# Performance work log

Measured on AMD Instinct MI355X. Metric: run time of the kernel, lower is better.

The kernel has to match this reference:

```python
import jax, jax.numpy as jnp
import numpy as np

N_NODES = 100000
N_EDGES = 3200000  # avg degree 32
D_IN = 128
D_OUT = 64
BN_EPS = 0.001


def setup_inputs() -> dict:
    key = jax.random.key(0)
    k1, k2, k3, k4, k5 = jax.random.split(key, 5)
    x = jax.random.normal(k1, (N_NODES, D_IN), dtype=jnp.float32)
    W = jax.random.normal(k2, (D_IN, D_OUT), dtype=jnp.float32) * 0.05
    edge_val = jax.random.uniform(k3, (N_EDGES,), dtype=jnp.float32)
    edge_src = jax.random.randint(k4, (N_EDGES,), 0, N_NODES, dtype=jnp.int32)
    edge_dst = jax.random.randint(k5, (N_EDGES,), 0, N_NODES, dtype=jnp.int32)
    return {"x": x, "W": W, "edge_val": edge_val,
            "edge_src": edge_src, "edge_dst": edge_dst}


def reference(x, W, edge_val, edge_src, edge_dst):
    # pre_sup = X @ W  (dense feature transform; dropout rate is 0 -> identity)
    pre_sup = x @ W  # [N, D_OUT]
    # support = A @ pre_sup, A given in COO form: A[dst, src] = edge_val
    msgs = edge_val[:, None] * pre_sup[edge_src]          # [E, D_OUT]
    out = jax.ops.segment_sum(msgs, edge_dst, num_segments=N_NODES)  # [N, D_OUT]
    # tf.nn.moments over all-but-last axis + batch_norm (no scale/offset, eps=1e-3)
    mean = jnp.mean(out, axis=0)
    var = jnp.var(out, axis=0)
    out = (out - mean) * jax.lax.rsqrt(var + BN_EPS)
    return jax.nn.relu(out)
```

## Files before the change

kernel.cpp:

```cpp
#include <hip/hip_runtime.h>
#include <stdint.h>

#define D_IN  128
#define D_OUT 64
#define BN_EPS 1e-3f

#define BIN_SHIFT 6
#define BIN_NODES 64
#define BIN_CAP   2560
#define CHUNK     8192
#define MAX_BINS  1600
#define STAT_SLICES 64

typedef __attribute__((ext_vector_type(8))) short bf16x8;
typedef __attribute__((ext_vector_type(4))) float f32x4;

__device__ __forceinline__ ushort f32_to_bf16_rne(float f) {
  uint u = __float_as_uint(f);
  u += 0x7FFFu + ((u >> 16) & 1u);
  return (ushort)(u >> 16);
}
__device__ __forceinline__ float bf16_to_f32(ushort h) {
  return __uint_as_float((uint)h << 16);
}

__global__ __launch_bounds__(256) void gemm_mfma_kernel(
    const float* __restrict__ x, const float* __restrict__ W,
    ushort* __restrict__ pre16, int n_nodes, int n_tiles) {
  __shared__ ushort Wb[D_IN * D_OUT];
  const int t = threadIdx.x;
  for (int i = t; i < D_IN * D_OUT; i += 256) Wb[i] = f32_to_bf16_rne(W[i]);
  __syncthreads();

  const int lane = t & 63;
  const int wave = t >> 6;
  const int m = lane & 15;
  const int quad = lane >> 4;

  bf16x8 bfrag[4][4];
#pragma unroll
  for (int nt = 0; nt < 4; ++nt)
#pragma unroll
    for (int s = 0; s < 4; ++s)
#pragma unroll
      for (int j = 0; j < 8; ++j)
        bfrag[nt][s][j] =
            (short)Wb[(32 * s + quad * 8 + j) * D_OUT + nt * 16 + m];

  for (int tile = blockIdx.x; tile < n_tiles; tile += gridDim.x) {
    const int rbase = tile * 64 + wave * 16;
    const int row = rbase + m;
    const size_t rl = (size_t)min(row, n_nodes - 1);
    f32x4 acc0 = {0.f, 0.f, 0.f, 0.f}, acc1 = {0.f, 0.f, 0.f, 0.f};
    f32x4 acc2 = {0.f, 0.f, 0.f, 0.f}, acc3 = {0.f, 0.f, 0.f, 0.f};
#pragma unroll
    for (int s = 0; s < 4; ++s) {
      const float4 xa = *(const float4*)&x[rl * D_IN + s * 32 + quad * 8];
      const float4 xb = *(const float4*)&x[rl * D_IN + s * 32 + quad * 8 + 4];
      bf16x8 af;
      af[0] = (short)f32_to_bf16_rne(xa.x);
      af[1] = (short)f32_to_bf16_rne(xa.y);
      af[2] = (short)f32_to_bf16_rne(xa.z);
      af[3] = (short)f32_to_bf16_rne(xa.w);
      af[4] = (short)f32_to_bf16_rne(xb.x);
      af[5] = (short)f32_to_bf16_rne(xb.y);
      af[6] = (short)f32_to_bf16_rne(xb.z);
      af[7] = (short)f32_to_bf16_rne(xb.w);
      acc0 = __builtin_amdgcn_mfma_f32_16x16x32_bf16(af, bfrag[0][s], acc0, 0, 0, 0);
      acc1 = __builtin_amdgcn_mfma_f32_16x16x32_bf16(af, bfrag[1][s], acc1, 0, 0, 0);
      acc2 = __builtin_amdgcn_mfma_f32_16x16x32_bf16(af, bfrag[2][s], acc2, 0, 0, 0);
      acc3 = __builtin_amdgcn_mfma_f32_16x16x32_bf16(af, bfrag[3][s], acc3, 0, 0, 0);
    }
#pragma unroll
    for (int reg = 0; reg < 4; ++reg) {
      const int r = rbase + quad * 4 + reg;
      if (r < n_nodes) {
        ushort* po = &pre16[(size_t)r * D_OUT + m];
        po[0]  = f32_to_bf16_rne(acc0[reg]);
        po[16] = f32_to_bf16_rne(acc1[reg]);
        po[32] = f32_to_bf16_rne(acc2[reg]);
        po[48] = f32_to_bf16_rne(acc3[reg]);
      }
    }
  }
}

__global__ __launch_bounds__(256) void partition_kernel(
    const float* __restrict__ ev, const int* __restrict__ esrc,
    const int* __restrict__ edst, int* __restrict__ bin_cursor,
    uint2* __restrict__ bucket, int n_edges, int n_bins) {
  __shared__ int cnt[MAX_BINS];
  __shared__ int base[MAX_BINS];
  const int t = threadIdx.x;
  const int beg = blockIdx.x * CHUNK;
  const int end = min(beg + CHUNK, n_edges);

  for (int i = t; i < n_bins; i += 256) cnt[i] = 0;
  __syncthreads();

  for (int i = beg + t * 4; i < end; i += 1024) {
    if (i + 3 < end) {
      const int4 d4 = *(const int4*)&edst[i];
      atomicAdd(&cnt[d4.x >> BIN_SHIFT], 1);
      atomicAdd(&cnt[d4.y >> BIN_SHIFT], 1);
      atomicAdd(&cnt[d4.z >> BIN_SHIFT], 1);
      atomicAdd(&cnt[d4.w >> BIN_SHIFT], 1);
    } else {
      for (int k = i; k < end; ++k) atomicAdd(&cnt[edst[k] >> BIN_SHIFT], 1);
    }
  }
  __syncthreads();

  for (int i = t; i < n_bins; i += 256) {
    const int c = cnt[i];
    int b = 0;
    if (c > 0) b = atomicAdd(&bin_cursor[i], c);
    if (b > BIN_CAP) b = BIN_CAP;
    base[i] = i * BIN_CAP + b;
    cnt[i] = 0;
  }
  __syncthreads();

  for (int i = beg + t * 4; i < end; i += 1024) {
    if (i + 3 < end) {
      const int4 d4 = *(const int4*)&edst[i];
      const int4 s4 = *(const int4*)&esrc[i];
      const float4 v4 = *(const float4*)&ev[i];
#pragma unroll
      for (int k = 0; k < 4; ++k) {
        const int dst = (&d4.x)[k];
        const int src = (&s4.x)[k];
        const float v = (&v4.x)[k];
        const int bin = dst >> BIN_SHIFT;
        const int r = atomicAdd(&cnt[bin], 1);
        const int pos = base[bin] + r;
        if (pos < (bin + 1) * BIN_CAP) {
          const uint w0 = ((uint)(dst & (BIN_NODES - 1)) << 17) | (uint)src;
          bucket[pos] = make_uint2(w0, __float_as_uint(v));
        }
      }
    } else {
      for (int k = i; k < end; ++k) {
        const int dst = edst[k];
        const int bin = dst >> BIN_SHIFT;
        const int r = atomicAdd(&cnt[bin], 1);
        const int pos = base[bin] + r;
        if (pos < (bin + 1) * BIN_CAP) {
          const uint w0 = ((uint)(dst & (BIN_NODES - 1)) << 17) | (uint)esrc[k];
          bucket[pos] = make_uint2(w0, __float_as_uint(ev[k]));
        }
      }
    }
  }
}

__global__ __launch_bounds__(256) void bin_sort_kernel(
    uint2* __restrict__ bucket, const int* __restrict__ bin_cursor,
    int2* __restrict__ seg, int n_nodes) {
  __shared__ uint s_src[BIN_CAP];
  __shared__ uint s_val[BIN_CAP];
  __shared__ int s_hist[BIN_NODES];
  __shared__ int s_off[BIN_NODES + 1];
  __shared__ int s_cur[BIN_NODES];

  const int t = threadIdx.x;
  const int bin = blockIdx.x;
  const int cnt = min(bin_cursor[bin], BIN_CAP);
  const int64_t rbase = (int64_t)bin * BIN_CAP;

  if (t < BIN_NODES) s_hist[t] = 0;
  __syncthreads();

  for (int i = t; i < cnt; i += 256)
    atomicAdd(&s_hist[bucket[rbase + i].x >> 17], 1);
  __syncthreads();

  int own = (t < BIN_NODES) ? s_hist[t] : 0;
  for (int off = 1; off < BIN_NODES; off <<= 1) {
    int u = 0;
    if (t < BIN_NODES && t >= off) u = s_hist[t - off];
    __syncthreads();
    if (t < BIN_NODES) s_hist[t] += u;
    __syncthreads();
  }
  if (t < BIN_NODES) {
    const int e = s_hist[t] - own;
    s_off[t] = e;
    s_cur[t] = e;
  }
  if (t == 0) s_off[BIN_NODES] = cnt;
  __syncthreads();

  for (int i = t; i < cnt; i += 256) {
    const uint2 r = bucket[rbase + i];
    const int d = r.x >> 17;
    const int p = atomicAdd(&s_cur[d], 1);
    s_src[p] = r.x & 0x1FFFFu;
    s_val[p] = r.y;
  }
  __syncthreads();

  for (int i = t; i < cnt; i += 256)
    bucket[rbase + i] = make_uint2(s_src[i], s_val[i]);

  if (t < BIN_NODES) {
    const int node = bin * BIN_NODES + t;
    if (node < n_nodes)
      seg[node] = make_int2((int)rbase + s_off[t], (int)rbase + s_off[t + 1]);
  }
}

__global__ __launch_bounds__(256) void gather_kernel(
    const ushort* __restrict__ pre16, const uint2* __restrict__ srec,
    const int2* __restrict__ seg, float* __restrict__ out,
    float* __restrict__ stats, int n_nodes) {
  __shared__ float red[4 * 64];
  __shared__ float red2[4 * 64];

  const int t = threadIdx.x;
  const int lane = t & 63;
  const int wave = t >> 6;
  const int half = lane >> 5;
  const int hl = lane & 31;
  const int node = blockIdx.x * 4 + wave;
  float csx = 0.f, csy = 0.f, cs2x = 0.f, cs2y = 0.f;

  if (node < n_nodes) {
    const int2 se = seg[node];
    const int je = se.y;
    float a0x = 0.f, a0y = 0.f, a1x = 0.f, a1y = 0.f;
    float a2x = 0.f, a2y = 0.f, a3x = 0.f, a3y = 0.f;
    float a4x = 0.f, a4y = 0.f, a5x = 0.f, a5y = 0.f;
    float a6x = 0.f, a6y = 0.f, a7x = 0.f, a7y = 0.f;
    int j = se.x + half;
    for (; j + 14 < je; j += 16) {
      const uint2 r0 = srec[j],      r1 = srec[j + 2];
      const uint2 r2 = srec[j + 4],  r3 = srec[j + 6];
      const uint2 r4 = srec[j + 8],  r5 = srec[j + 10];
      const uint2 r6 = srec[j + 12], r7 = srec[j + 14];
      const uint p0 = *(const uint*)&pre16[(size_t)r0.x * D_OUT + 2 * hl];
      const uint p1 = *(const uint*)&pre16[(size_t)r1.x * D_OUT + 2 * hl];
      const uint p2 = *(const uint*)&pre16[(size_t)r2.x * D_OUT + 2 * hl];
      const uint p3 = *(const uint*)&pre16[(size_t)r3.x * D_OUT + 2 * hl];
      const uint p4 = *(const uint*)&pre16[(size_t)r4.x * D_OUT + 2 * hl];
      const uint p5 = *(const uint*)&pre16[(size_t)r5.x * D_OUT + 2 * hl];
      const uint p6 = *(const uint*)&pre16[(size_t)r6.x * D_OUT + 2 * hl];
      const uint p7 = *(const uint*)&pre16[(size_t)r7.x * D_OUT + 2 * hl];
      const float v0 = __uint_as_float(r0.y), v1 = __uint_as_float(r1.y);
      const float v2 = __uint_as_float(r2.y), v3 = __uint_as_float(r3.y);
      const float v4 = __uint_as_float(r4.y), v5 = __uint_as_float(r5.y);
      const float v6 = __uint_as_float(r6.y), v7 = __uint_as_float(r7.y);
      a0x += v0 * bf16_to_f32((ushort)(p0 & 0xFFFFu));
      a0y += v0 * bf16_to_f32((ushort)(p0 >> 16));
      a1x += v1 * bf16_to_f32((ushort)(p1 & 0xFFFFu));
      a1y += v1 * bf16_to_f32((ushort)(p1 >> 16));
      a2x += v2 * bf16_to_f32((ushort)(p2 & 0xFFFFu));
      a2y += v2 * bf16_to_f32((ushort)(p2 >> 16));
      a3x += v3 * bf16_to_f32((ushort)(p3 & 0xFFFFu));
      a3y += v3 * bf16_to_f32((ushort)(p3 >> 16));
      a4x += v4 * bf16_to_f32((ushort)(p4 & 0xFFFFu));
      a4y += v4 * bf16_to_f32((ushort)(p4 >> 16));
      a5x += v5 * bf16_to_f32((ushort)(p5 & 0xFFFFu));
      a5y += v5 * bf16_to_f32((ushort)(p5 >> 16));
      a6x += v6 * bf16_to_f32((ushort)(p6 & 0xFFFFu));
      a6y += v6 * bf16_to_f32((ushort)(p6 >> 16));
      a7x += v7 * bf16_to_f32((ushort)(p7 & 0xFFFFu));
      a7y += v7 * bf16_to_f32((ushort)(p7 >> 16));
    }
    for (; j + 6 < je; j += 8) {
      const uint2 r0 = srec[j],     r1 = srec[j + 2];
      const uint2 r2 = srec[j + 4], r3 = srec[j + 6];
      const uint p0 = *(const uint*)&pre16[(size_t)r0.x * D_OUT + 2 * hl];
      const uint p1 = *(const uint*)&pre16[(size_t)r1.x * D_OUT + 2 * hl];
      const uint p2 = *(const uint*)&pre16[(size_t)r2.x * D_OUT + 2 * hl];
      const uint p3 = *(const uint*)&pre16[(size_t)r3.x * D_OUT + 2 * hl];
      const float v0 = __uint_as_float(r0.y), v1 = __uint_as_float(r1.y);
      const float v2 = __uint_as_float(r2.y), v3 = __uint_as_float(r3.y);
      a0x += v0 * bf16_to_f32((ushort)(p0 & 0xFFFFu));
      a0y += v0 * bf16_to_f32((ushort)(p0 >> 16));
      a1x += v1 * bf16_to_f32((ushort)(p1 & 0xFFFFu));
      a1y += v1 * bf16_to_f32((ushort)(p1 >> 16));
      a2x += v2 * bf16_to_f32((ushort)(p2 & 0xFFFFu));
      a2y += v2 * bf16_to_f32((ushort)(p2 >> 16));
      a3x += v3 * bf16_to_f32((ushort)(p3 & 0xFFFFu));
      a3y += v3 * bf16_to_f32((ushort)(p3 >> 16));
    }
    for (; j < je; j += 2) {
      const uint2 r = srec[j];
      const float v = __uint_as_float(r.y);
      const uint p = *(const uint*)&pre16[(size_t)r.x * D_OUT + 2 * hl];
      a0x += v * bf16_to_f32((ushort)(p & 0xFFFFu));
      a0y += v * bf16_to_f32((ushort)(p >> 16));
    }
    float ax = ((a0x + a1x) + (a2x + a3x)) + ((a4x + a5x) + (a6x + a7x));
    float ay = ((a0y + a1y) + (a2y + a3y)) + ((a4y + a5y) + (a6y + a7y));
    ax += __shfl_xor(ax, 32);
    ay += __shfl_xor(ay, 32);
    if (half == 0) {
      *(float2*)&out[(size_t)node * D_OUT + 2 * hl] = make_float2(ax, ay);
      csx = ax;
      cs2x = ax * ax;
      csy = ay;
      cs2y = ay * ay;
    }
  }

  if (half == 0) {
    red[wave * 64 + 2 * hl] = csx;
    red[wave * 64 + 2 * hl + 1] = csy;
    red2[wave * 64 + 2 * hl] = cs2x;
    red2[wave * 64 + 2 * hl + 1] = cs2y;
  }
  __syncthreads();
  if (t < 64) {
    const float s = red[t] + red[64 + t] + red[128 + t] + red[192 + t];
    const float s2 = red2[t] + red2[64 + t] + red2[128 + t] + red2[192 + t];
    const int sl = (blockIdx.x & (STAT_SLICES - 1)) * 128;
    atomicAdd(&stats[sl + t], s);
    atomicAdd(&stats[sl + 64 + t], s2);
  }
}

__global__ __launch_bounds__(128) void stats_reduce_kernel(
    const float* __restrict__ stats, float* __restrict__ sfinal) {
  const int c = threadIdx.x;
  float s = 0.f;
#pragma unroll 8
  for (int sl = 0; sl < STAT_SLICES; ++sl) s += stats[sl * 128 + c];
  sfinal[c] = s;
}

__global__ __launch_bounds__(256) void norm_kernel(
    float* __restrict__ out, const float* __restrict__ stats, int64_t n_vec4,
    float inv_n) {
  const int c = (threadIdx.x * 4) & 63;
  float mean[4], scale[4];
#pragma unroll
  for (int k = 0; k < 4; ++k) {
    mean[k] = stats[c + k] * inv_n;
    const float var = stats[64 + c + k] * inv_n - mean[k] * mean[k];
    scale[k] = rsqrtf(var + BN_EPS);
  }
  const int64_t stride = (int64_t)gridDim.x * 256;
  for (int64_t i = (int64_t)blockIdx.x * 256 + threadIdx.x; i < n_vec4;
       i += stride) {
    float4 v = ((float4*)out)[i];
    v.x = (v.x - mean[0]) * scale[0];
    v.y = (v.y - mean[1]) * scale[1];
    v.z = (v.z - mean[2]) * scale[2];
    v.w = (v.w - mean[3]) * scale[3];
    v.x = v.x > 0.f ? v.x : 0.f;
    v.y = v.y > 0.f ? v.y : 0.f;
    v.z = v.z > 0.f ? v.z : 0.f;
    v.w = v.w > 0.f ? v.w : 0.f;
    ((float4*)out)[i] = v;
  }
}

extern "C" void kernel_launch(void* const* d_in, const int* in_sizes, int n_in,
                              void* d_out, int out_size, void* d_ws,
                              size_t ws_size, hipStream_t stream) {
  const float* x = (const float*)d_in[0];
  const float* W = (const float*)d_in[1];
  const float* ev = (const float*)d_in[2];
  const int* esrc = (const int*)d_in[3];
  const int* edst = (const int*)d_in[4];

  const int n_nodes = in_sizes[0] / D_IN;
  const int n_edges = in_sizes[2];
  const int64_t n_out = (int64_t)n_nodes * D_OUT;
  const int n_bins = (n_nodes + BIN_NODES - 1) >> BIN_SHIFT;
  const int n_row_tiles = (n_nodes + 63) / 64;

  float* out = (float*)d_out;

  char* w = (char*)d_ws;
  ushort* pre16 = (ushort*)w;             w += (size_t)n_nodes * D_OUT * 2;
  int* bin_cursor = (int*)w;              w += (size_t)n_bins * 4;
  float* stats = (float*)w;               w += (size_t)STAT_SLICES * 128 * 4;
  float* sfinal = (float*)w;              w += 128 * 4;
  w = (char*)(((uintptr_t)w + 7) & ~(uintptr_t)7);
  int2* seg = (int2*)w;                   w += (size_t)n_nodes * 8;
  uint2* bucket = (uint2*)w;

  hipMemsetAsync(bin_cursor, 0, (size_t)n_bins * 4, stream);
  hipMemsetAsync(stats, 0, (size_t)STAT_SLICES * 128 * 4, stream);

  gemm_mfma_kernel<<<(n_row_tiles + 1) / 2, 256, 0, stream>>>(
      x, W, pre16, n_nodes, n_row_tiles);
  partition_kernel<<<(n_edges + CHUNK - 1) / CHUNK, 256, 0, stream>>>(
      ev, esrc, edst, bin_cursor, bucket, n_edges, n_bins);
  bin_sort_kernel<<<n_bins, 256, 0, stream>>>(bucket, bin_cursor, seg, n_nodes);
  gather_kernel<<<(n_nodes + 3) / 4, 256, 0, stream>>>(pre16, bucket, seg, out,
                                                       stats, n_nodes);
  stats_reduce_kernel<<<1, 128, 0, stream>>>(stats, sfinal);
  norm_kernel<<<2048, 256, 0, stream>>>(out, sfinal, n_out / 4,
                                        1.0f / (float)n_nodes);
}
```

Measured before the change: 316.8 us.

## Replace bin partition/sort with global CSR build via degree count, scan, scatter

Replaces the two-pass binned partition and per-bin LDS sort with a global CSR construction: per-node degree atomics, a three-kernel prefix scan, and an atomic-cursor scatter of edge records. This removes the fixed bin capacity and the in-shared-memory sort. In exchange it adds launches and per-edge global atomics with random scattered stores. The GEMM epilogue also stages results through shared memory so pre16 rows are written with wide coalesced stores.

```diff
diff --git a/kernel.cpp b/kernel.cpp
--- a/kernel.cpp
+++ b/kernel.cpp
@@ -5,12 +5,9 @@
 #define D_OUT 64
 #define BN_EPS 1e-3f
 
-#define BIN_SHIFT 6
-#define BIN_NODES 64
-#define BIN_CAP   2560
-#define CHUNK     8192
-#define MAX_BINS  1600
 #define STAT_SLICES 64
+#define PT_STRIDE 72
+#define SCAN_CHUNK 1024
 
 typedef __attribute__((ext_vector_type(8))) short bf16x8;
 typedef __attribute__((ext_vector_type(4))) float f32x4;
@@ -28,6 +25,7 @@
     const float* __restrict__ x, const float* __restrict__ W,
     ushort* __restrict__ pre16, int n_nodes, int n_tiles) {
   __shared__ ushort Wb[D_IN * D_OUT];
+  __shared__ ushort ptile[64 * PT_STRIDE];
   const int t = threadIdx.x;
   for (int i = t; i < D_IN * D_OUT; i += 256) Wb[i] = f32_to_bf16_rne(W[i]);
   __syncthreads();
@@ -48,8 +46,8 @@
             (short)Wb[(32 * s + quad * 8 + j) * D_OUT + nt * 16 + m];
 
   for (int tile = blockIdx.x; tile < n_tiles; tile += gridDim.x) {
-    const int rbase = tile * 64 + wave * 16;
-    const int row = rbase + m;
+    const int rbase0 = tile * 64;
+    const int row = rbase0 + wave * 16 + m;
     const size_t rl = (size_t)min(row, n_nodes - 1);
     f32x4 acc0 = {0.f, 0.f, 0.f, 0.f}, acc1 = {0.f, 0.f, 0.f, 0.f};
     f32x4 acc2 = {0.f, 0.f, 0.f, 0.f}, acc3 = {0.f, 0.f, 0.f, 0.f};
@@ -71,148 +69,129 @@
       acc2 = __builtin_amdgcn_mfma_f32_16x16x32_bf16(af, bfrag[2][s], acc2, 0, 0, 0);
       acc3 = __builtin_amdgcn_mfma_f32_16x16x32_bf16(af, bfrag[3][s], acc3, 0, 0, 0);
     }
+    __syncthreads();
 #pragma unroll
     for (int reg = 0; reg < 4; ++reg) {
-      const int r = rbase + quad * 4 + reg;
+      const int lr = wave * 16 + quad * 4 + reg;
+      ptile[lr * PT_STRIDE + m]      = f32_to_bf16_rne(acc0[reg]);
+      ptile[lr * PT_STRIDE + 16 + m] = f32_to_bf16_rne(acc1[reg]);
+      ptile[lr * PT_STRIDE + 32 + m] = f32_to_bf16_rne(acc2[reg]);
+      ptile[lr * PT_STRIDE + 48 + m] = f32_to_bf16_rne(acc3[reg]);
+    }
+    __syncthreads();
+    {
+      const int lr = t >> 2;
+      const int sg = t & 3;
+      const int r = rbase0 + lr;
       if (r < n_nodes) {
-        ushort* po = &pre16[(size_t)r * D_OUT + m];
-        po[0]  = f32_to_bf16_rne(acc0[reg]);
-        po[16] = f32_to_bf16_rne(acc1[reg]);
-        po[32] = f32_to_bf16_rne(acc2[reg]);
-        po[48] = f32_to_bf16_rne(acc3[reg]);
+        const uint4* pl = (const uint4*)&ptile[lr * PT_STRIDE + sg * 16];
+        uint4* po = (uint4*)&pre16[(size_t)r * D_OUT + sg * 16];
+        po[0] = pl[0];
+        po[1] = pl[1];
       }
     }
   }
 }
 
-__global__ __launch_bounds__(256) void partition_kernel(
+__global__ __launch_bounds__(256) void degree_kernel(
+    const int* __restrict__ edst, int* __restrict__ deg, int n_edges) {
+  const int g = blockIdx.x * 256 + threadIdx.x;
+  const int n4 = n_edges >> 2;
+  const int stride = gridDim.x * 256;
+  for (int i = g; i < n4; i += stride) {
+    const int4 d4 = ((const int4*)edst)[i];
+    atomicAdd(&deg[d4.x], 1);
+    atomicAdd(&deg[d4.y], 1);
+    atomicAdd(&deg[d4.z], 1);
+    atomicAdd(&deg[d4.w], 1);
+  }
+  const int idx = (n4 << 2) + g;
+  if (idx < n_edges) atomicAdd(&deg[edst[idx]], 1);
+}
+
+__global__ __launch_bounds__(256) void scan1_kernel(
+    const int* __restrict__ deg, int* __restrict__ row_start,
+    int* __restrict__ chunk_sums, int n_nodes) {
+  __shared__ int sdata[256];
+  const int t = threadIdx.x;
+  const int base = blockIdx.x * SCAN_CHUNK + t * 4;
+  int d[4];
+#pragma unroll
+  for (int k = 0; k < 4; ++k) d[k] = (base + k < n_nodes) ? deg[base + k] : 0;
+  const int s = d[0] + d[1] + d[2] + d[3];
+  sdata[t] = s;
+  __syncthreads();
+  for (int off = 1; off < 256; off <<= 1) {
+    const int u = (t >= off) ? sdata[t - off] : 0;
+    __syncthreads();
+    sdata[t] += u;
+    __syncthreads();
+  }
+  int run = sdata[t] - s;
+#pragma unroll
+  for (int k = 0; k < 4; ++k) {
+    if (base + k < n_nodes) row_start[base + k] = run;
+    run += d[k];
+  }
+  if (t == 255) chunk_sums[blockIdx.x] = sdata[255];
+}
+
+__global__ __launch_bounds__(1024) void scan2_kernel(
+    const int* __restrict__ chunk_sums, int* __restrict__ chunk_offs,
+    int n_chunks) {
+  __shared__ int sdata[1024];
+  const int t = threadIdx.x;
+  const int v = (t < n_chunks) ? chunk_sums[t] : 0;
+  sdata[t] = v;
+  __syncthreads();
+  for (int off = 1; off < 1024; off <<= 1) {
+    const int u = (t >= off) ? sdata[t - off] : 0;
+    __syncthreads();
+    sdata[t] += u;
+    __syncthreads();
+  }
+  if (t < n_chunks) chunk_offs[t] = sdata[t] - v;
+}
+
+__global__ __launch_bounds__(256) void scan3_kernel(
+    int* __restrict__ row_start, int* __restrict__ cur,
+    const int* __restrict__ chunk_offs, int n_nodes, int n_edges) {
+  const int i = blockIdx.x * 256 + threadIdx.x;
+  if (i < n_nodes) {
+    const int v = row_start[i] + chunk_offs[i >> 10];
+    row_start[i] = v;
+    cur[i] = v;
+  }
+  if (i == 0) row_start[n_nodes] = n_edges;
+}
+
+__global__ __launch_bounds__(256) void scatter_kernel(
     const float* __restrict__ ev, const int* __restrict__ esrc,
-    const int* __restrict__ edst, int* __restrict__ bin_cursor,
-    uint2* __restrict__ bucket, int n_edges, int n_bins) {
-  __shared__ int cnt[MAX_BINS];
-  __shared__ int base[MAX_BINS];
-  const int t = threadIdx.x;
-  const int beg = blockIdx.x * CHUNK;
-  const int end = min(beg + CHUNK, n_edges);
-
-  for (int i = t; i < n_bins; i += 256) cnt[i] = 0;
-  __syncthreads();
-
-  for (int i = beg + t * 4; i < end; i += 1024) {
-    if (i + 3 < end) {
-      const int4 d4 = *(const int4*)&edst[i];
-      atomicAdd(&cnt[d4.x >> BIN_SHIFT], 1);
-      atomicAdd(&cnt[d4.y >> BIN_SHIFT], 1);
-      atomicAdd(&cnt[d4.z >> BIN_SHIFT], 1);
-      atomicAdd(&cnt[d4.w >> BIN_SHIFT], 1);
-    } else {
-      for (int k = i; k < end; ++k) atomicAdd(&cnt[edst[k] >> BIN_SHIFT], 1);
-    }
-  }
-  __syncthreads();
-
-  for (int i = t; i < n_bins; i += 256) {
-    const int c = cnt[i];
-    int b = 0;
-    if (c > 0) b = atomicAdd(&bin_cursor[i], c);
-    if (b > BIN_CAP) b = BIN_CAP;
-    base[i] = i * BIN_CAP + b;
-    cnt[i] = 0;
-  }
-  __syncthreads();
-
-  for (int i = beg + t * 4; i < end; i += 1024) {
-    if (i + 3 < end) {
-      const int4 d4 = *(const int4*)&edst[i];
-      const int4 s4 = *(const int4*)&esrc[i];
-      const float4 v4 = *(const float4*)&ev[i];
-#pragma unroll
-      for (int k = 0; k < 4; ++k) {
-        const int dst = (&d4.x)[k];
-        const int src = (&s4.x)[k];
-        const float v = (&v4.x)[k];
-        const int bin = dst >> BIN_SHIFT;
-        const int r = atomicAdd(&cnt[bin], 1);
-        const int pos = base[bin] + r;
-        if (pos < (bin + 1) * BIN_CAP) {
-          const uint w0 = ((uint)(dst & (BIN_NODES - 1)) << 17) | (uint)src;
-          bucket[pos] = make_uint2(w0, __float_as_uint(v));
-        }
-      }
-    } else {
-      for (int k = i; k < end; ++k) {
-        const int dst = edst[k];
-        const int bin = dst >> BIN_SHIFT;
-        const int r = atomicAdd(&cnt[bin], 1);
-        const int pos = base[bin] + r;
-        if (pos < (bin + 1) * BIN_CAP) {
-          const uint w0 = ((uint)(dst & (BIN_NODES - 1)) << 17) | (uint)esrc[k];
-          bucket[pos] = make_uint2(w0, __float_as_uint(ev[k]));
-        }
-      }
-    }
-  }
-}
-
-__global__ __launch_bounds__(256) void bin_sort_kernel(
-    uint2* __restrict__ bucket, const int* __restrict__ bin_cursor,
-    int2* __restrict__ seg, int n_nodes) {
-  __shared__ uint s_src[BIN_CAP];
-  __shared__ uint s_val[BIN_CAP];
-  __shared__ int s_hist[BIN_NODES];
-  __shared__ int s_off[BIN_NODES + 1];
-  __shared__ int s_cur[BIN_NODES];
-
-  const int t = threadIdx.x;
-  const int bin = blockIdx.x;
-  const int cnt = min(bin_cursor[bin], BIN_CAP);
-  const int64_t rbase = (int64_t)bin * BIN_CAP;
-
-  if (t < BIN_NODES) s_hist[t] = 0;
-  __syncthreads();
-
-  for (int i = t; i < cnt; i += 256)
-    atomicAdd(&s_hist[bucket[rbase + i].x >> 17], 1);
-  __syncthreads();
-
-  int own = (t < BIN_NODES) ? s_hist[t] : 0;
-  for (int off = 1; off < BIN_NODES; off <<= 1) {
-    int u = 0;
-    if (t < BIN_NODES && t >= off) u = s_hist[t - off];
-    __syncthreads();
-    if (t < BIN_NODES) s_hist[t] += u;
-    __syncthreads();
-  }
-  if (t < BIN_NODES) {
-    const int e = s_hist[t] - own;
-    s_off[t] = e;
-    s_cur[t] = e;
-  }
-  if (t == 0) s_off[BIN_NODES] = cnt;
-  __syncthreads();
-
-  for (int i = t; i < cnt; i += 256) {
-    const uint2 r = bucket[rbase + i];
-    const int d = r.x >> 17;
-    const int p = atomicAdd(&s_cur[d], 1);
-    s_src[p] = r.x & 0x1FFFFu;
-    s_val[p] = r.y;
-  }
-  __syncthreads();
-
-  for (int i = t; i < cnt; i += 256)
-    bucket[rbase + i] = make_uint2(s_src[i], s_val[i]);
-
-  if (t < BIN_NODES) {
-    const int node = bin * BIN_NODES + t;
-    if (node < n_nodes)
-      seg[node] = make_int2((int)rbase + s_off[t], (int)rbase + s_off[t + 1]);
+    const int* __restrict__ edst, int* __restrict__ cur,
+    uint2* __restrict__ bucket, int n_edges) {
+  const int g = blockIdx.x * 256 + threadIdx.x;
+  const int n4 = n_edges >> 2;
+  const int stride = gridDim.x * 256;
+  for (int i = g; i < n4; i += stride) {
+    const int4 d4 = ((const int4*)edst)[i];
+    const int4 s4 = ((const int4*)esrc)[i];
+    const float4 v4 = ((const float4*)ev)[i];
+#pragma unroll
+    for (int k = 0; k < 4; ++k) {
+      const int pos = atomicAdd(&cur[(&d4.x)[k]], 1);
+      bucket[pos] = make_uint2((uint)(&s4.x)[k], __float_as_uint((&v4.x)[k]));
+    }
+  }
+  const int idx = (n4 << 2) + g;
+  if (idx < n_edges) {
+    const int pos = atomicAdd(&cur[edst[idx]], 1);
+    bucket[pos] = make_uint2((uint)esrc[idx], __float_as_uint(ev[idx]));
   }
 }
 
 __global__ __launch_bounds__(256) void gather_kernel(
     const ushort* __restrict__ pre16, const uint2* __restrict__ srec,
-    const int2* __restrict__ seg, float* __restrict__ out,
+    const int* __restrict__ row_start, float* __restrict__ out,
     float* __restrict__ stats, int n_nodes) {
   __shared__ float red[4 * 64];
   __shared__ float red2[4 * 64];
@@ -226,13 +205,13 @@
   float csx = 0.f, csy = 0.f, cs2x = 0.f, cs2y = 0.f;
 
   if (node < n_nodes) {
-    const int2 se = seg[node];
-    const int je = se.y;
+    const int jb = row_start[node];
+    const int je = row_start[node + 1];
     float a0x = 0.f, a0y = 0.f, a1x = 0.f, a1y = 0.f;
     float a2x = 0.f, a2y = 0.f, a3x = 0.f, a3y = 0.f;
     float a4x = 0.f, a4y = 0.f, a5x = 0.f, a5y = 0.f;
     float a6x = 0.f, a6y = 0.f, a7x = 0.f, a7y = 0.f;
-    int j = se.x + half;
+    int j = jb + half;
     for (; j + 14 < je; j += 16) {
       const uint2 r0 = srec[j],      r1 = srec[j + 2];
       const uint2 r2 = srec[j + 4],  r3 = srec[j + 6];
@@ -369,30 +348,38 @@
   const int n_nodes = in_sizes[0] / D_IN;
   const int n_edges = in_sizes[2];
   const int64_t n_out = (int64_t)n_nodes * D_OUT;
-  const int n_bins = (n_nodes + BIN_NODES - 1) >> BIN_SHIFT;
   const int n_row_tiles = (n_nodes + 63) / 64;
+  const int n_chunks = (n_nodes + SCAN_CHUNK - 1) / SCAN_CHUNK;
 
   float* out = (float*)d_out;
 
   char* w = (char*)d_ws;
   ushort* pre16 = (ushort*)w;             w += (size_t)n_nodes * D_OUT * 2;
-  int* bin_cursor = (int*)w;              w += (size_t)n_bins * 4;
+  int* deg = (int*)w;                     w += (size_t)n_nodes * 4;
+  int* cur = (int*)w;                     w += (size_t)n_nodes * 4;
+  int* row_start = (int*)w;               w += (size_t)(n_nodes + 1) * 4;
+  int* chunk_sums = (int*)w;              w += 1024 * 4;
+  int* chunk_offs = (int*)w;              w += 1024 * 4;
   float* stats = (float*)w;               w += (size_t)STAT_SLICES * 128 * 4;
   float* sfinal = (float*)w;              w += 128 * 4;
   w = (char*)(((uintptr_t)w + 7) & ~(uintptr_t)7);
-  int2* seg = (int2*)w;                   w += (size_t)n_nodes * 8;
   uint2* bucket = (uint2*)w;
 
-  hipMemsetAsync(bin_cursor, 0, (size_t)n_bins * 4, stream);
+  hipMemsetAsync(deg, 0, (size_t)n_nodes * 4, stream);
   hipMemsetAsync(stats, 0, (size_t)STAT_SLICES * 128 * 4, stream);
 
   gemm_mfma_kernel<<<(n_row_tiles + 1) / 2, 256, 0, stream>>>(
       x, W, pre16, n_nodes, n_row_tiles);
-  partition_kernel<<<(n_edges + CHUNK - 1) / CHUNK, 256, 0, stream>>>(
-      ev, esrc, edst, bin_cursor, bucket, n_edges, n_bins);
-  bin_sort_kernel<<<n_bins, 256, 0, stream>>>(bucket, bin_cursor, seg, n_nodes);
-  gather_kernel<<<(n_nodes + 3) / 4, 256, 0, stream>>>(pre16, bucket, seg, out,
-                                                       stats, n_nodes);
+  degree_kernel<<<1024, 256, 0, stream>>>(edst, deg, n_edges);
+  scan1_kernel<<<n_chunks, 256, 0, stream>>>(deg, row_start, chunk_sums,
+                                             n_nodes);
+  scan2_kernel<<<1, 1024, 0, stream>>>(chunk_sums, chunk_offs, n_chunks);
+  scan3_kernel<<<(n_nodes + 255) / 256, 256, 0, stream>>>(
+      row_start, cur, chunk_offs, n_nodes, n_edges);
+  scatter_kernel<<<1024, 256, 0, stream>>>(ev, esrc, edst, cur, bucket,
+                                           n_edges);
+  gather_kernel<<<(n_nodes + 3) / 4, 256, 0, stream>>>(pre16, bucket, row_start,
+                                                       out, stats, n_nodes);
   stats_reduce_kernel<<<1, 128, 0, stream>>>(stats, sfinal);
   norm_kernel<<<2048, 256, 0, stream>>>(out, sfinal, n_out / 4,
                                         1.0f / (float)n_nodes);
```

Result: slower. 578.7 us (+82.6%).
